# Performance work log

Measured on AMD Instinct MI355X. Metric: run time of the kernel, lower is better.

The kernel has to match this reference:

```python
import jax, jax.numpy as jnp
import numpy as np

RADIUS = 4
NUM_LEVELS = 4
STRIDES = (1, 1, 1, 1)


def _level_corr(f1, f2, coords, r, stride):
    """Windowed bilinear correlation at one pyramid level.
    f1: [B,C,H,W] (full-res features), f2: [B,C,H2,W2] (level features),
    coords: [B,2,H,W] (x,y) already scaled to f2's resolution.
    Returns [B,(2r+1)^2,H,W].
    """
    B, C, H, W = f1.shape
    H2, W2 = f2.shape[2], f2.shape[3]
    f1t = jnp.transpose(f1, (0, 2, 3, 1))                     # [B,H,W,C]
    f2f = jnp.transpose(f2, (0, 2, 3, 1)).reshape(B, H2 * W2, C)
    d = jnp.arange(-r, r + 1, dtype=f1.dtype) * stride
    dy, dx = jnp.meshgrid(d, d, indexing='ij')
    deltas = jnp.stack([dx.ravel(), dy.ravel()], axis=-1)      # [(2r+1)^2, 2]

    def one_offset(delta):
        x = coords[:, 0] + delta[0]                            # [B,H,W]
        y = coords[:, 1] + delta[1]
        x0 = jnp.floor(x)
        y0 = jnp.floor(y)
        acc = jnp.zeros((B, H, W), f1.dtype)
        # 4 bilinear corners, zero padding outside the feature map
        for cx in (0.0, 1.0):
            for cy in (0.0, 1.0):
                xc = x0 + cx
                yc = y0 + cy
                w = (1.0 - jnp.abs(x - xc)) * (1.0 - jnp.abs(y - yc))
                valid = (xc >= 0) & (xc <= W2 - 1) & (yc >= 0) & (yc <= H2 - 1)
                idx = (jnp.clip(yc, 0, H2 - 1) * W2 + jnp.clip(xc, 0, W2 - 1)).astype(jnp.int32)
                g = jax.vmap(lambda t, i: t[i])(f2f, idx.reshape(B, -1)).reshape(B, H, W, C)
                acc = acc + jnp.where(valid, w, 0.0) * jnp.einsum('bhwc,bhwc->bhw', f1t, g)
        return acc                                             # [B,H,W]

    corr = jax.lax.map(one_offset, deltas)                     # [K,B,H,W]
    return jnp.transpose(corr, (1, 0, 2, 3))                   # [B,K,H,W]


def _corr_block(fmap1, fmap2s, coords):
    C = fmap1.shape[1]
    outs = []
    for i, f2 in enumerate(fmap2s):
        outs.append(_level_corr(fmap1, f2, coords / (2.0 ** i), RADIUS, STRIDES[i]))
    corr = jnp.concatenate(outs, axis=1)                       # [B, L*(2r+1)^2, H, W]
    return corr / jnp.sqrt(jnp.asarray(C, fmap1.dtype))


def setup_inputs() -> dict:
    key = jax.random.key(0)
    ks = jax.random.split(key, 6)
    B, C, H, W = 2, 256, 64, 64
    inp = {'fmap1': jax.random.normal(ks[0], (B, C, H, W), jnp.float32)}
    for i in range(NUM_LEVELS):
        h, w = H >> i, W >> i
        inp['fmap2_%d' % i] = jax.random.normal(ks[1 + i], (B, C, h, w), jnp.float32)
    gy, gx = jnp.meshgrid(jnp.arange(H, dtype=jnp.float32), jnp.arange(W, dtype=jnp.float32), indexing='ij')
    base = jnp.broadcast_to(jnp.stack([gx, gy], 0)[None], (B, 2, H, W))
    flow = 2.0 * jax.random.normal(jax.random.fold_in(key, 99), (B, 2, H, W), jnp.float32)
    inp['coords'] = base + flow
    return inp


def reference(fmap1, fmap2_0, fmap2_1, fmap2_2, fmap2_3, coords):
    return _corr_block(fmap1, [fmap2_0, fmap2_1, fmap2_2, fmap2_3], coords)
```

## Files before the change

kernel.cpp:

```cpp
#include <hip/hip_runtime.h>

#define RADIUS 4
#define KK 81
#define HWP 4096

typedef _Float16 f16x8 __attribute__((ext_vector_type(8)));
typedef float    f32x4 __attribute__((ext_vector_type(4)));

#define OFF_F1T  0u
#define OFF_L0   4194304u
#define OFF_L1   8388608u
#define OFF_L2   9437184u
#define OFF_L3   9699328u
#define OFF_ZPAD 9764864u
#define OFF_END  9765376u

__global__ __launch_bounds__(256) void stage_kernel(
    const float* __restrict__ f1, const float* __restrict__ l0,
    const float* __restrict__ l1, const float* __restrict__ l2,
    const float* __restrict__ l3, char* __restrict__ wsB)
{
    __shared__ float tile[32][33];
    const int bx = blockIdx.x;
    const int b  = blockIdx.z;
    const int r0 = blockIdx.y * 32;
    const int tx = threadIdx.x, ty = threadIdx.y;
    if (bx == 0 && blockIdx.y == 0 && b == 0) {
        const int tt = ty * 32 + tx;
        if (tt < 128) ((float*)(wsB + OFF_ZPAD))[tt] = 0.0f;
    }
    const float* src; _Float16* dst; int S, s0i;
    if (bx < 128)      { src = f1; dst = (_Float16*)(wsB + OFF_F1T); S = 4096; s0i = bx; }
    else if (bx < 256) { src = l0; dst = (_Float16*)(wsB + OFF_L0);  S = 4096; s0i = bx - 128; }
    else if (bx < 288) { src = l1; dst = (_Float16*)(wsB + OFF_L1);  S = 1024; s0i = bx - 256; }
    else if (bx < 296) { src = l2; dst = (_Float16*)(wsB + OFF_L2);  S = 256;  s0i = bx - 288; }
    else               { src = l3; dst = (_Float16*)(wsB + OFF_L3);  S = 64;   s0i = bx - 296; }
    const int s0 = s0i * 32;
    src += (size_t)b * 256 * S;
    dst += (size_t)b * S * 256;
    #pragma unroll
    for (int i = 0; i < 32; i += 8)
        tile[ty + i][tx] = src[(size_t)(r0 + ty + i) * S + s0 + tx];
    __syncthreads();
    #pragma unroll
    for (int i = 0; i < 32; i += 8)
        dst[(size_t)(s0 + ty + i) * 256 + r0 + tx] = (_Float16)tile[tx][ty + i];
}

__global__ __launch_bounds__(256, 3) void corr_mfma_kernel(
    const char* __restrict__ wsB,
    const float* __restrict__ coords,
    float* __restrict__ out)
{
    __shared__ f32x4 sB[2][1024];
    __shared__ float sD[32][104];
    __shared__ int   sIx[32], sIy[32];
    __shared__ float sW[32][4];
    __shared__ int   sBox[5];

    char* sBb = (char*)sB;

    const int bx   = blockIdx.x;
    const int lvl  = blockIdx.y;
    const int tile = ((bx & 7) << 5) | (bx >> 3);
    const int b    = tile >> 7;
    const int t7   = tile & 127;
    const int tr4  = (t7 >> 3) << 2;
    const int tc8  = (t7 & 7) << 3;
    const int t    = threadIdx.x;
    const int l    = t & 63;
    const int wid  = t >> 6;
    const int aset = wid & 1;
    const int half = wid >> 1;

    const int sh = 6 - lvl;
    const int W2 = 1 << sh;

    for (int i = t; i < 32 * 104; i += 256)
        ((float*)sD)[i] = 0.0f;

    if (t < 32) {
        const int hwc = ((tr4 + (t >> 3)) << 6) + tc8 + (t & 7);
        const float sc = 1.0f / (float)(1 << lvl);
        const float xs = coords[((size_t)b * 2 + 0) * HWP + hwc] * sc;
        const float ys = coords[((size_t)b * 2 + 1) * HWP + hwc] * sc;
        const float x0f = floorf(xs), y0f = floorf(ys);
        sIx[t] = (int)x0f; sIy[t] = (int)y0f;
        const float fx = xs - x0f, fy = ys - y0f;
        sW[t][0] = (1.f - fx) * (1.f - fy);
        sW[t][1] = fx * (1.f - fy);
        sW[t][2] = (1.f - fx) * fy;
        sW[t][3] = fx * fy;
    }
    __syncthreads();
    if (t == 0) {
        int rlo = 1 << 20, rhi = -(1 << 20), clo = 1 << 20, chi = -(1 << 20);
        for (int px = 0; px < 32; ++px) {
            rlo = min(rlo, sIy[px]); rhi = max(rhi, sIy[px]);
            clo = min(clo, sIx[px]); chi = max(chi, sIx[px]);
        }
        const int rl = max(rlo - RADIUS, 0);
        const int rh = min(rhi + RADIUS + 1, W2 - 1);
        const int cf = max(clo - RADIUS, 0);
        const int ce = min(chi + RADIUS + 1, W2 - 1);
        const int nr = rh - rl + 1;
        const int nt = (ce >= cf) ? ((ce - cf + 16) >> 4) : 0;
        sBox[0] = rl;
        sBox[1] = cf;
        sBox[2] = nt;
        sBox[3] = (nr > 0) ? nr * nt : 0;
        sBox[4] = 65535 / max(nt, 1) + 1;
    }

    const int pxl = (aset << 4) + (l & 15);
    const int hwA = ((tr4 + (pxl >> 3)) << 6) + tc8 + (pxl & 7);
    const char* ap = wsB + OFF_F1T + ((size_t)(b * HWP + hwA)) * 512 + ((l >> 4) << 4);
    const f16x8 a0 = __builtin_bit_cast(f16x8, *(const f32x4*)(ap));
    const f16x8 a1 = __builtin_bit_cast(f16x8, *(const f32x4*)(ap + 64));
    const f16x8 a2 = __builtin_bit_cast(f16x8, *(const f32x4*)(ap + 128));
    const f16x8 a3 = __builtin_bit_cast(f16x8, *(const f32x4*)(ap + 192));
    const f16x8 a4 = __builtin_bit_cast(f16x8, *(const f32x4*)(ap + 256));
    const f16x8 a5 = __builtin_bit_cast(f16x8, *(const f32x4*)(ap + 320));
    const f16x8 a6 = __builtin_bit_cast(f16x8, *(const f32x4*)(ap + 384));
    const f16x8 a7 = __builtin_bit_cast(f16x8, *(const f32x4*)(ap + 448));
    __syncthreads();

    const int rlo = sBox[0], cfi = sBox[1], ntw = sBox[2];
    const int ntot = sBox[3], inv = sBox[4];
    const int NP = (ntot + 1) >> 1;
    const unsigned lvbase = ((lvl == 0) ? OFF_L0 : (lvl == 1) ? OFF_L1
                           : (lvl == 2) ? OFF_L2 : OFF_L3)
                          + (((unsigned)b << (2 * sh)) << 9);
    const int coff = l & 15;

    const int pxg  = (aset << 4) + ((l >> 4) << 2);
    const int iy0r = sIy[pxg + 0], ix0r = sIx[pxg + 0];
    const int iy1r = sIy[pxg + 1], ix1r = sIx[pxg + 1];
    const int iy2r = sIy[pxg + 2], ix2r = sIx[pxg + 2];
    const int iy3r = sIy[pxg + 3], ix3r = sIx[pxg + 3];

#define LOADP(P_, R0_, R1_, R2_, R3_) { \
        const int u_ = ((P_) << 1) + (t >> 7); \
        const unsigned q_ = ((unsigned)(u_ * inv)) >> 16; \
        const int j_ = u_ - (int)q_ * ntw; \
        const int col_ = cfi + (j_ << 4) + (t & 15); \
        const bool ok_ = (u_ < ntot) && ((unsigned)col_ < (unsigned)W2); \
        const int row_ = rlo + (int)q_; \
        const char* gp_ = wsB + (ok_ ? (lvbase + ((unsigned)((row_ << sh) + col_) << 9)) \
                                     : OFF_ZPAD) + ((unsigned)((t >> 4) & 7) << 6); \
        R0_ = *(const f32x4*)(gp_); \
        R1_ = *(const f32x4*)(gp_ + 16); \
        R2_ = *(const f32x4*)(gp_ + 32); \
        R3_ = *(const f32x4*)(gp_ + 48); \
        __builtin_amdgcn_sched_barrier(0); }

#define WRITEP(BUF_, R0_, R1_, R2_, R3_) { \
        char* wp_ = sBb + ((BUF_) << 14) + ((t >> 7) << 13) + (((t >> 4) & 7) << 10) \
                  + ((t & 15) << 4); \
        *(f32x4*)(wp_)       = R0_; \
        *(f32x4*)(wp_ + 256) = R1_; \
        *(f32x4*)(wp_ + 512) = R2_; \
        *(f32x4*)(wp_ + 768) = R3_; }

#define CONSUMEP(BUF_, P_) { \
        const int u_ = ((P_) << 1) + half; \
        if (u_ < ntot) { \
            const unsigned q_ = ((unsigned)(u_ * inv)) >> 16; \
            const int j_ = u_ - (int)q_ * ntw; \
            const int row_ = rlo + (int)q_; \
            const char* lb_ = sBb + ((BUF_) << 14) + (half << 13) + ((l >> 4) << 8) \
                            + ((l & 15) << 4); \
            const f16x8 b0_ = __builtin_bit_cast(f16x8, *(const f32x4*)(lb_)); \
            const f16x8 b1_ = __builtin_bit_cast(f16x8, *(const f32x4*)(lb_ + 1024)); \
            const f16x8 b2_ = __builtin_bit_cast(f16x8, *(const f32x4*)(lb_ + 2048)); \
            const f16x8 b3_ = __builtin_bit_cast(f16x8, *(const f32x4*)(lb_ + 3072)); \
            const f16x8 b4_ = __builtin_bit_cast(f16x8, *(const f32x4*)(lb_ + 4096)); \
            const f16x8 b5_ = __builtin_bit_cast(f16x8, *(const f32x4*)(lb_ + 5120)); \
            const f16x8 b6_ = __builtin_bit_cast(f16x8, *(const f32x4*)(lb_ + 6144)); \
            const f16x8 b7_ = __builtin_bit_cast(f16x8, *(const f32x4*)(lb_ + 7168)); \
            f32x4 ac0 = {0.f, 0.f, 0.f, 0.f}; \
            f32x4 ac1 = {0.f, 0.f, 0.f, 0.f}; \
            ac0 = __builtin_amdgcn_mfma_f32_16x16x32_f16(a0, b0_, ac0, 0, 0, 0); \
            ac1 = __builtin_amdgcn_mfma_f32_16x16x32_f16(a1, b1_, ac1, 0, 0, 0); \
            ac0 = __builtin_amdgcn_mfma_f32_16x16x32_f16(a2, b2_, ac0, 0, 0, 0); \
            ac1 = __builtin_amdgcn_mfma_f32_16x16x32_f16(a3, b3_, ac1, 0, 0, 0); \
            ac0 = __builtin_amdgcn_mfma_f32_16x16x32_f16(a4, b4_, ac0, 0, 0, 0); \
            ac1 = __builtin_amdgcn_mfma_f32_16x16x32_f16(a5, b5_, ac1, 0, 0, 0); \
            ac0 = __builtin_amdgcn_mfma_f32_16x16x32_f16(a6, b6_, ac0, 0, 0, 0); \
            ac1 = __builtin_amdgcn_mfma_f32_16x16x32_f16(a7, b7_, ac1, 0, 0, 0); \
            const f32x4 accs = ac0 + ac1; \
            const int col_ = cfi + (j_ << 4) + coff; \
            const int p0 = row_ - iy0r + RADIUS, q0 = col_ - ix0r + RADIUS; \
            if ((unsigned)p0 < 10u && (unsigned)q0 < 10u) sD[pxg + 0][p0 * 10 + q0] = accs[0]; \
            const int p1 = row_ - iy1r + RADIUS, q1 = col_ - ix1r + RADIUS; \
            if ((unsigned)p1 < 10u && (unsigned)q1 < 10u) sD[pxg + 1][p1 * 10 + q1] = accs[1]; \
            const int p2 = row_ - iy2r + RADIUS, q2 = col_ - ix2r + RADIUS; \
            if ((unsigned)p2 < 10u && (unsigned)q2 < 10u) sD[pxg + 2][p2 * 10 + q2] = accs[2]; \
            const int p3 = row_ - iy3r + RADIUS, q3 = col_ - ix3r + RADIUS; \
            if ((unsigned)p3 < 10u && (unsigned)q3 < 10u) sD[pxg + 3][p3 * 10 + q3] = accs[3]; \
        } }

    {
        f32x4 XA, XB, XC, XD, YA, YB, YC, YD;
        if (ntot > 0) {
            LOADP(0, XA, XB, XC, XD);
            if (NP > 1) LOADP(1, YA, YB, YC, YD);
            WRITEP(0, XA, XB, XC, XD);
        }
        __syncthreads();
        if (ntot > 0) {
            int p = 0;
            for (;;) {
                if (p + 2 < NP) LOADP(p + 2, XA, XB, XC, XD);
                CONSUMEP(p & 1, p);
                if (p + 1 < NP) WRITEP((p + 1) & 1, YA, YB, YC, YD);
                __syncthreads();
                if (++p >= NP) break;
                if (p + 2 < NP) LOADP(p + 2, YA, YB, YC, YD);
                CONSUMEP(p & 1, p);
                if (p + 1 < NP) WRITEP((p + 1) & 1, XA, XB, XC, XD);
                __syncthreads();
                if (++p >= NP) break;
            }
        }
    }
#undef LOADP
#undef WRITEP
#undef CONSUMEP
    __syncthreads();

    for (int j = t; j < 32 * KK; j += 256) {
        const int px = j & 31;
        const int k  = j >> 5;
        const int p  = (k * 57) >> 9;
        const int q  = k - p * 9;
        const int bi = p * 10 + q;
        const float* dd = sD[px];
        const float v = (sW[px][0] * dd[bi]      + sW[px][1] * dd[bi + 1] +
                         sW[px][2] * dd[bi + 10] + sW[px][3] * dd[bi + 11]) * 0.0625f;
        const int hwp = ((tr4 + (px >> 3)) << 6) + tc8 + (px & 7);
        out[((size_t)b * 324 + lvl * KK + k) * HWP + hwp] = v;
    }
}

__global__ __launch_bounds__(128) void corr_level_kernel(
    const float* __restrict__ f1, const float* __restrict__ f2,
    const float* __restrict__ coords, float* __restrict__ out,
    int H2, int W2, float scale, int lvl)
{
    __shared__ float sf1[256];
    __shared__ float sDl[100];
    const int pix = blockIdx.x;
    const int b   = pix >> 12;
    const int hw  = pix & 4095;
    const int t   = threadIdx.x;
    for (int c = t; c < 256; c += 128)
        sf1[c] = f1[((size_t)b * 256 + c) * 4096 + hw];
    __syncthreads();
    const float xs = coords[((size_t)b * 2 + 0) * 4096 + hw] * scale;
    const float ys = coords[((size_t)b * 2 + 1) * 4096 + hw] * scale;
    const float x0f = floorf(xs), y0f = floorf(ys);
    const float fx = xs - x0f, fy = ys - y0f;
    const int ix0 = (int)x0f, iy0 = (int)y0f;
    if (t < 100) {
        const int p = t / 10, q = t - p * 10;
        const int row = iy0 - 4 + p, col = ix0 - 4 + q;
        float acc = 0.0f;
        if (row >= 0 && row < H2 && col >= 0 && col < W2) {
            const size_t step = (size_t)H2 * W2;
            const size_t base = (size_t)b * 256 * step + (size_t)row * W2 + col;
            #pragma unroll 4
            for (int c = 0; c < 256; ++c)
                acc += f2[base + (size_t)c * step] * sf1[c];
        }
        sDl[t] = acc;
    }
    __syncthreads();
    if (t < 81) {
        const int p = t / 9, q = t - p * 9;
        const float d00 = sDl[p * 10 + q];
        const float d01 = sDl[p * 10 + q + 1];
        const float d10 = sDl[p * 10 + q + 10];
        const float d11 = sDl[p * 10 + q + 11];
        const float v = (1.0f - fy) * ((1.0f - fx) * d00 + fx * d01)
                      + fy * ((1.0f - fx) * d10 + fx * d11);
        out[((size_t)b * 324 + (size_t)lvl * 81 + t) * 4096 + hw] = v * 0.0625f;
    }
}

extern "C" void kernel_launch(void* const* d_in, const int* in_sizes, int n_in,
                              void* d_out, int out_size, void* d_ws, size_t ws_size,
                              hipStream_t stream) {
    (void)out_size;
    const float* f1     = (const float*)d_in[0];
    const float* f2l[4] = {(const float*)d_in[1], (const float*)d_in[2],
                           (const float*)d_in[3], (const float*)d_in[4]};
    const float* coords = (const float*)d_in[5];

    {
        int nbig = 0;
        for (int i = 0; i < n_in; ++i) {
            const int sz = in_sizes[i];
            if (sz == 2097152) {
                if (nbig == 0) f1 = (const float*)d_in[i];
                else           f2l[0] = (const float*)d_in[i];
                ++nbig;
            }
            else if (sz == 524288) f2l[1] = (const float*)d_in[i];
            else if (sz == 131072) f2l[2] = (const float*)d_in[i];
            else if (sz ==  32768) f2l[3] = (const float*)d_in[i];
            else if (sz ==  16384) coords = (const float*)d_in[i];
        }
    }
    float* out = (float*)d_out;
    char*  wsB = (char*)d_ws;

    if (ws_size >= (size_t)OFF_END) {
        stage_kernel<<<dim3(298, 8, 2), dim3(32, 8, 1), 0, stream>>>(
            f1, f2l[0], f2l[1], f2l[2], f2l[3], wsB);
        corr_mfma_kernel<<<dim3(256, 4, 1), 256, 0, stream>>>(wsB, coords, out);
    } else {
        for (int lvl = 0; lvl < 4; ++lvl) {
            const int W2 = 64 >> lvl;
            const float scale = 1.0f / (float)(1 << lvl);
            corr_level_kernel<<<8192, 128, 0, stream>>>(
                f1, f2l[lvl], coords, out, W2, W2, scale, lvl);
        }
    }
}
```

Baseline: 44.53 us.

## Vectorize staging transpose and replace syncthreads with LDS-only barriers

The staging transpose kernel now has each thread load a float4 row segment and store four fp16 channels as one 8-byte write, in a 1D 256-thread block with a padded tile. This cuts the number of global memory instructions. In the correlation kernel, every __syncthreads is replaced by a barrier that waits only on LDS counters (lgkmcnt), so in-flight global prefetch loads are not drained at each barrier. This relies on the register prefetch being correctly ordered without a vmcnt wait, and the padded tile reads may cause LDS bank conflicts.

```diff
diff --git a/kernel.cpp b/kernel.cpp
--- a/kernel.cpp
+++ b/kernel.cpp
@@ -5,6 +5,7 @@
 #define HWP 4096
 
 typedef _Float16 f16x8 __attribute__((ext_vector_type(8)));
+typedef _Float16 f16x4 __attribute__((ext_vector_type(4)));
 typedef float    f32x4 __attribute__((ext_vector_type(4)));
 
 #define OFF_F1T  0u
@@ -20,15 +21,13 @@
     const float* __restrict__ l1, const float* __restrict__ l2,
     const float* __restrict__ l3, char* __restrict__ wsB)
 {
-    __shared__ float tile[32][33];
+    __shared__ float tile[32][36];
     const int bx = blockIdx.x;
     const int b  = blockIdx.z;
     const int r0 = blockIdx.y * 32;
-    const int tx = threadIdx.x, ty = threadIdx.y;
-    if (bx == 0 && blockIdx.y == 0 && b == 0) {
-        const int tt = ty * 32 + tx;
-        if (tt < 128) ((float*)(wsB + OFF_ZPAD))[tt] = 0.0f;
-    }
+    const int t  = threadIdx.x;
+    if (bx == 0 && blockIdx.y == 0 && b == 0 && t < 128)
+        ((float*)(wsB + OFF_ZPAD))[t] = 0.0f;
     const float* src; _Float16* dst; int S, s0i;
     if (bx < 128)      { src = f1; dst = (_Float16*)(wsB + OFF_F1T); S = 4096; s0i = bx; }
     else if (bx < 256) { src = l0; dst = (_Float16*)(wsB + OFF_L0);  S = 4096; s0i = bx - 128; }
@@ -38,14 +37,26 @@
     const int s0 = s0i * 32;
     src += (size_t)b * 256 * S;
     dst += (size_t)b * S * 256;
-    #pragma unroll
-    for (int i = 0; i < 32; i += 8)
-        tile[ty + i][tx] = src[(size_t)(r0 + ty + i) * S + s0 + tx];
+    {
+        const int row = t >> 3, cg = t & 7;
+        *(f32x4*)&tile[row][cg * 4] =
+            *(const f32x4*)&src[(size_t)(r0 + row) * S + s0 + cg * 4];
+    }
     __syncthreads();
-    #pragma unroll
-    for (int i = 0; i < 32; i += 8)
-        dst[(size_t)(s0 + ty + i) * 256 + r0 + tx] = (_Float16)tile[tx][ty + i];
+    {
+        const int sidx = t >> 3, chg = t & 7;
+        f16x4 o;
+        o[0] = (_Float16)tile[chg * 4 + 0][sidx];
+        o[1] = (_Float16)tile[chg * 4 + 1][sidx];
+        o[2] = (_Float16)tile[chg * 4 + 2][sidx];
+        o[3] = (_Float16)tile[chg * 4 + 3][sidx];
+        *(f16x4*)&dst[(size_t)(s0 + sidx) * 256 + r0 + chg * 4] = o;
+    }
 }
+
+#define BARRIER_LW { asm volatile("s_waitcnt lgkmcnt(0)" ::: "memory"); \
+                     __builtin_amdgcn_s_barrier(); \
+                     __builtin_amdgcn_sched_barrier(0); }
 
 __global__ __launch_bounds__(256, 3) void corr_mfma_kernel(
     const char* __restrict__ wsB,
@@ -92,7 +103,7 @@
         sW[t][2] = (1.f - fx) * fy;
         sW[t][3] = fx * fy;
     }
-    __syncthreads();
+    BARRIER_LW;
     if (t == 0) {
         int rlo = 1 << 20, rhi = -(1 << 20), clo = 1 << 20, chi = -(1 << 20);
         for (int px = 0; px < 32; ++px) {
@@ -123,7 +134,7 @@
     const f16x8 a5 = __builtin_bit_cast(f16x8, *(const f32x4*)(ap + 320));
     const f16x8 a6 = __builtin_bit_cast(f16x8, *(const f32x4*)(ap + 384));
     const f16x8 a7 = __builtin_bit_cast(f16x8, *(const f32x4*)(ap + 448));
-    __syncthreads();
+    BARRIER_LW;
 
     const int rlo = sBox[0], cfi = sBox[1], ntw = sBox[2];
     const int ntot = sBox[3], inv = sBox[4];
@@ -207,19 +218,19 @@
             if (NP > 1) LOADP(1, YA, YB, YC, YD);
             WRITEP(0, XA, XB, XC, XD);
         }
-        __syncthreads();
+        BARRIER_LW;
         if (ntot > 0) {
             int p = 0;
             for (;;) {
                 if (p + 2 < NP) LOADP(p + 2, XA, XB, XC, XD);
                 CONSUMEP(p & 1, p);
                 if (p + 1 < NP) WRITEP((p + 1) & 1, YA, YB, YC, YD);
-                __syncthreads();
+                BARRIER_LW;
                 if (++p >= NP) break;
                 if (p + 2 < NP) LOADP(p + 2, YA, YB, YC, YD);
                 CONSUMEP(p & 1, p);
                 if (p + 1 < NP) WRITEP((p + 1) & 1, XA, XB, XC, XD);
-                __syncthreads();
+                BARRIER_LW;
                 if (++p >= NP) break;
             }
         }
@@ -227,7 +238,7 @@
 #undef LOADP
 #undef WRITEP
 #undef CONSUMEP
-    __syncthreads();
+    BARRIER_LW;
 
     for (int j = t; j < 32 * KK; j += 256) {
         const int px = j & 31;
@@ -316,7 +327,7 @@
     char*  wsB = (char*)d_ws;
 
     if (ws_size >= (size_t)OFF_END) {
-        stage_kernel<<<dim3(298, 8, 2), dim3(32, 8, 1), 0, stream>>>(
+        stage_kernel<<<dim3(298, 8, 2), dim3(256, 1, 1), 0, stream>>>(
             f1, f2l[0], f2l[1], f2l[2], f2l[3], wsB);
         corr_mfma_kernel<<<dim3(256, 4, 1), 256, 0, stream>>>(wsB, coords, out);
     } else {
```

New measurement: 44.92 us. About the same (+0.9%).
